# Kernel optimization log

Measured on AMD Instinct MI355X. Metric: run time of the kernel, lower is better.

## Reference

```python
import jax, jax.numpy as jnp
import numpy as np

EPS = 1e-7
LN_EPS = 1e-5

N_NODES = 50000
N_EDGES = 1600000
D = 128
L = 3


def layer_norm(h, scale, bias):
    mu = jnp.mean(h, axis=-1, keepdims=True)
    var = jnp.var(h, axis=-1, keepdims=True)
    return (h - mu) * jax.lax.rsqrt(var + LN_EPS) * scale + bias


def gen_conv(h, src, dst, edge_attr, W1, b1, W2, b2, beta, n_nodes):
    # message: ReLU(x_j + edge_attr) + eps   -> [E, D]
    msg = jax.nn.relu(h[src] + edge_attr) + EPS
    # softmax aggregation over incoming edges of each dst node, per feature
    s = beta * msg
    m = jax.ops.segment_max(s, dst, num_segments=n_nodes)  # [N, D]
    e = jnp.exp(s - m[dst])
    den = jax.ops.segment_sum(e, dst, num_segments=n_nodes)  # [N, D]
    alpha = e / den[dst]
    aggr = jax.ops.segment_sum(alpha * msg, dst, num_segments=n_nodes)  # [N, D]
    # MLP(x + aggr): D -> 2D -> D
    out = h + aggr
    out = jax.nn.relu(out @ W1 + b1)
    return out @ W2 + b2


def setup_inputs() -> dict:
    key = jax.random.key(0)
    ks = jax.random.split(key, 8)
    x = jax.random.normal(ks[0], (N_NODES, D), dtype=jnp.float32)
    edge_index = jax.random.randint(ks[1], (2, N_EDGES), 0, N_NODES, dtype=jnp.int64)
    edge_attr = jax.random.normal(ks[2], (N_EDGES, D), dtype=jnp.float32)
    return {
        "x": x,
        "edge_index": edge_index,
        "edge_attr": edge_attr,
        "ln_scale": jnp.ones((L, D), jnp.float32),
        "ln_bias": jnp.zeros((L, D), jnp.float32),
        "W1": jax.random.normal(ks[3], (L, D, 2 * D), jnp.float32) * 0.05,
        "b1": jnp.zeros((L, 2 * D), jnp.float32),
        "W2": jax.random.normal(ks[4], (L, 2 * D, D), jnp.float32) * 0.05,
        "b2": jnp.zeros((L, D), jnp.float32),
        "beta": jnp.ones((L,), jnp.float32),
        "lnf_scale": jnp.ones((D,), jnp.float32),
        "lnf_bias": jnp.zeros((D,), jnp.float32),
        "Wout": jax.random.normal(ks[5], (D, 1), jnp.float32) * 0.05,
        "bout": jnp.zeros((1,), jnp.float32),
    }


def reference(x, edge_index, edge_attr, ln_scale, ln_bias, W1, b1, W2, b2, beta,
              lnf_scale, lnf_bias, Wout, bout):
    src, dst = edge_index[0], edge_index[1]
    n = x.shape[0]
    # res+ DeeperGCN: first conv raw, then LN -> ReLU -> conv + residual
    h = gen_conv(x, src, dst, edge_attr, W1[0], b1[0], W2[0], b2[0], beta[0], n)
    for i in range(1, L):
        hn = jax.nn.relu(layer_norm(h, ln_scale[i], ln_bias[i]))
        h = gen_conv(hn, src, dst, edge_attr, W1[i], b1[i], W2[i], b2[i], beta[i], n) + h
    h = jax.nn.relu(layer_norm(h, lnf_scale, lnf_bias))
    return h @ Wout + bout
```

## Files before the change

kernel.cpp:

```cpp
#include <hip/hip_runtime.h>
#include <hip/hip_bf16.h>
#include <cstddef>

#define N_NODES 50000
#define N_EDGES 1600000
#define D 128
#define TWO_D 256
#define L 3
#define EPS 1e-7f
#define LN_EPS 1e-5f

typedef __attribute__((ext_vector_type(8))) short short8;
typedef __attribute__((ext_vector_type(4))) float f32x4;
typedef __attribute__((ext_vector_type(4))) unsigned u32x4;

__device__ __forceinline__ unsigned short f2bf(float f) {
    unsigned u = __float_as_uint(f);
    unsigned r = (u + 0x7fffu + ((u >> 16) & 1u)) >> 16;
    return (unsigned short)r;
}
__device__ __forceinline__ float bflo(unsigned u) { return __uint_as_float(u << 16); }
__device__ __forceinline__ float bfhi(unsigned u) { return __uint_as_float(u & 0xffff0000u); }
__device__ __forceinline__ unsigned bfpack(float lo, float hi) {
    return (unsigned)f2bf(lo) | ((unsigned)f2bf(hi) << 16);
}


__global__ __launch_bounds__(256) void hist_kernel(const int* __restrict__ ei, int* __restrict__ deg) {
    int idx = blockIdx.x * blockDim.x + threadIdx.x;
    int stride = gridDim.x * blockDim.x;
    for (int e = idx; e < N_EDGES; e += stride)
        atomicAdd(&deg[ei[N_EDGES + e]], 1);
}

__global__ __launch_bounds__(256) void scanA_kernel(const int* __restrict__ deg, int* __restrict__ part,
                                                    int* __restrict__ bsum) {
    __shared__ int wsum[4];
    int b = blockIdx.x, t = threadIdx.x;
    int lane = t & 63, wid = t >> 6;
    int base = b * 1024 + t * 4;
    int v0 = 0, v1 = 0, v2 = 0, v3 = 0;
    if (base + 0 < N_NODES) v0 = deg[base + 0];
    if (base + 1 < N_NODES) v1 = deg[base + 1];
    if (base + 2 < N_NODES) v2 = deg[base + 2];
    if (base + 3 < N_NODES) v3 = deg[base + 3];
    int s0 = v0, s1 = s0 + v1, s2 = s1 + v2, s3 = s2 + v3;
    int inc = s3;
    for (int off = 1; off < 64; off <<= 1) {
        int u = __shfl_up(inc, off);
        if (lane >= off) inc += u;
    }
    if (lane == 63) wsum[wid] = inc;
    __syncthreads();
    int woff = 0;
    for (int w = 0; w < wid; ++w) woff += wsum[w];
    int excl = woff + inc - s3;
    if (base + 0 < N_NODES) part[base + 0] = excl + s0;
    if (base + 1 < N_NODES) part[base + 1] = excl + s1;
    if (base + 2 < N_NODES) part[base + 2] = excl + s2;
    if (base + 3 < N_NODES) part[base + 3] = excl + s3;
    if (t == 255) bsum[b] = woff + inc;
}

__global__ __launch_bounds__(64) void scanB_kernel(int* __restrict__ bsum, int nb) {
    int lane = threadIdx.x;
    int v = (lane < nb) ? bsum[lane] : 0;
    int inc = v;
    for (int off = 1; off < 64; off <<= 1) {
        int u = __shfl_up(inc, off);
        if (lane >= off) inc += u;
    }
    if (lane < nb) bsum[lane] = inc - v;
}

__global__ __launch_bounds__(256) void scanC_kernel(const int* __restrict__ part, const int* __restrict__ bsum,
                                                    int* __restrict__ rowptr, int* __restrict__ cursor) {
    int i = blockIdx.x * blockDim.x + threadIdx.x;
    if (i >= N_NODES) return;
    rowptr[i + 1] = part[i] + bsum[i >> 10];
    cursor[i] = 0;
    if (i == 0) rowptr[0] = 0;
}

__global__ __launch_bounds__(256) void scatter_kernel(const int* __restrict__ ei, const int* __restrict__ rowptr,
                                                      int* __restrict__ cursor, int2* __restrict__ es2) {
    int idx = blockIdx.x * blockDim.x + threadIdx.x;
    int stride = gridDim.x * blockDim.x;
    for (int e = idx; e < N_EDGES; e += stride) {
        int dn = ei[N_EDGES + e];
        int pos = atomicAdd(&cursor[dn], 1);
        es2[rowptr[dn] + pos] = make_int2(ei[e], e);
    }
}

__global__ __launch_bounds__(256) void x2bf_kernel(const float* __restrict__ x, ushort2* __restrict__ xb) {
    int i = blockIdx.x * blockDim.x + threadIdx.x;
    if (i >= N_NODES * (D / 2)) return;
    float2 v = *(const float2*)(x + (size_t)i * 2);
    ushort2 o;
    o.x = f2bf(v.x);
    o.y = f2bf(v.y);
    xb[i] = o;
}

__global__ __launch_bounds__(256) void pack_w_kernel(const float* __restrict__ W1, const float* __restrict__ W2,
                                                     ushort* __restrict__ w1p, ushort* __restrict__ w2p) {
    int tid = blockIdx.x * 256 + threadIdx.x;
    if (tid >= 3 * 65536) return;
    int layer = tid >> 16, t2 = tid & 65535;
    if (t2 < 32768) {
        int j = t2 & 7, l = (t2 >> 3) & 63, kk = (t2 >> 9) & 3, ct = t2 >> 11;
        int k = kk * 32 + (l >> 4) * 8 + j, n = ct * 16 + (l & 15);
        w1p[(size_t)layer * 32768 + t2] = f2bf(W1[(size_t)layer * 32768 + k * 256 + n]);
    } else {
        int t3 = t2 - 32768;
        int j = t3 & 7, l = (t3 >> 3) & 63, kk = (t3 >> 9) & 7, ct = t3 >> 12;
        int k = kk * 32 + (l >> 4) * 8 + j, n = ct * 16 + (l & 15);
        w2p[(size_t)layer * 32768 + t3] = f2bf(W2[(size_t)layer * 32768 + k * 128 + n]);
    }
}


template <int PREP>
__global__ __launch_bounds__(256) void aggregate_kernel(const uint4* __restrict__ nodeb,
                                                        const float* __restrict__ ea,
                                                        ushort* __restrict__ eab,
                                                        const int* __restrict__ rowptr,
                                                        const int2* __restrict__ es2,
                                                        const float* __restrict__ beta, int layer,
                                                        ushort* __restrict__ preb) {
    int wid = threadIdx.x >> 6, lane = threadIdx.x & 63;
    int d = blockIdx.x * 4 + wid;
    if (d >= N_NODES) return;
    int e8 = lane >> 3;
    int f8 = lane & 7;
    float bet = beta[layer];
    int j0 = rowptr[d], j1 = rowptr[d + 1];
    int deg = j1 - j0;

    uint4 r0 = nodeb[(size_t)d * 16 + f8 * 2 + 0];
    uint4 r1 = nodeb[(size_t)d * 16 + f8 * 2 + 1];

    float se[16], sm[16];
#pragma unroll
    for (int i = 0; i < 16; ++i) { se[i] = 0.f; sm[i] = 0.f; }

    if (deg > 0) {
        int2 mp = (j0 + lane < j1) ? es2[j0 + lane] : make_int2(0, 0);
        bool small = (deg <= 64);
#pragma unroll 4
        for (int j = j0; j < j1; j += 8) {
            int e = j + e8;
            bool valid = e < j1;
            int ec = valid ? e : j1 - 1;
            int s, eid;
            if (small) {
                s   = __shfl(mp.x, ec - j0);
                eid = __shfl(mp.y, ec - j0);
            } else {
                int2 p = es2[ec];
                s = p.x; eid = p.y;
            }
            uint4 h0 = nodeb[(size_t)s * 16 + f8 * 2 + 0];
            uint4 h1 = nodeb[(size_t)s * 16 + f8 * 2 + 1];
            const unsigned* hu = (const unsigned*)&h0;
            const unsigned* hv = (const unsigned*)&h1;
            float vm = valid ? 1.f : 0.f;
            float af[16];
            if (PREP) {
                const float* ep = ea + (size_t)eid * D + f8 * 16;
                f32x4 fa0 = *(const f32x4*)(ep + 0);
                f32x4 fa1 = *(const f32x4*)(ep + 4);
                f32x4 fa2 = *(const f32x4*)(ep + 8);
                f32x4 fa3 = *(const f32x4*)(ep + 12);
#pragma unroll
                for (int q = 0; q < 4; ++q) {
                    af[q] = fa0[q];
                    af[4 + q] = fa1[q];
                    af[8 + q] = fa2[q];
                    af[12 + q] = fa3[q];
                }
                if (valid) {
                    u32x4 o0, o1;
                    o0[0] = bfpack(af[0], af[1]);  o0[1] = bfpack(af[2], af[3]);
                    o0[2] = bfpack(af[4], af[5]);  o0[3] = bfpack(af[6], af[7]);
                    o1[0] = bfpack(af[8], af[9]);  o1[1] = bfpack(af[10], af[11]);
                    o1[2] = bfpack(af[12], af[13]); o1[3] = bfpack(af[14], af[15]);
                    u32x4* dst = (u32x4*)(eab + (size_t)ec * D + f8 * 16);
                    dst[0] = o0;
                    dst[1] = o1;
                }
            } else {
                const u32x4* ap = (const u32x4*)(eab + (size_t)ec * D + f8 * 16);
                u32x4 a0 = ap[0];
                u32x4 a1 = ap[1];
#pragma unroll
                for (int q = 0; q < 4; ++q) {
                    af[q * 2 + 0] = bflo(a0[q]); af[q * 2 + 1] = bfhi(a0[q]);
                    af[8 + q * 2 + 0] = bflo(a1[q]); af[8 + q * 2 + 1] = bfhi(a1[q]);
                }
            }
#pragma unroll
            for (int q = 0; q < 4; ++q) {
                float m0 = fmaxf(bflo(hu[q]) + af[q * 2 + 0], 0.f) + EPS;
                float m1 = fmaxf(bfhi(hu[q]) + af[q * 2 + 1], 0.f) + EPS;
                float ee0 = __expf(bet * m0) * vm;
                float ee1 = __expf(bet * m1) * vm;
                se[q * 2 + 0] += ee0; sm[q * 2 + 0] = fmaf(ee0, m0, sm[q * 2 + 0]);
                se[q * 2 + 1] += ee1; sm[q * 2 + 1] = fmaf(ee1, m1, sm[q * 2 + 1]);
            }
#pragma unroll
            for (int q = 0; q < 4; ++q) {
                float m0 = fmaxf(bflo(hv[q]) + af[8 + q * 2 + 0], 0.f) + EPS;
                float m1 = fmaxf(bfhi(hv[q]) + af[8 + q * 2 + 1], 0.f) + EPS;
                float ee0 = __expf(bet * m0) * vm;
                float ee1 = __expf(bet * m1) * vm;
                se[8 + q * 2 + 0] += ee0; sm[8 + q * 2 + 0] = fmaf(ee0, m0, sm[8 + q * 2 + 0]);
                se[8 + q * 2 + 1] += ee1; sm[8 + q * 2 + 1] = fmaf(ee1, m1, sm[8 + q * 2 + 1]);
            }
        }
    }

#pragma unroll
    for (int off = 8; off < 64; off <<= 1) {
#pragma unroll
        for (int i = 0; i < 16; ++i) {
            se[i] += __shfl_xor(se[i], off);
            sm[i] += __shfl_xor(sm[i], off);
        }
    }

    if (e8 == 0) {
        const unsigned* ru = (const unsigned*)&r0;
        const unsigned* rv = (const unsigned*)&r1;
        float v[16];
#pragma unroll
        for (int q = 0; q < 4; ++q) {
            v[q * 2 + 0] = bflo(ru[q]) + (se[q * 2 + 0] > 0.f ? sm[q * 2 + 0] / se[q * 2 + 0] : 0.f);
            v[q * 2 + 1] = bfhi(ru[q]) + (se[q * 2 + 1] > 0.f ? sm[q * 2 + 1] / se[q * 2 + 1] : 0.f);
            v[8 + q * 2 + 0] = bflo(rv[q]) + (se[8 + q * 2 + 0] > 0.f ? sm[8 + q * 2 + 0] / se[8 + q * 2 + 0] : 0.f);
            v[8 + q * 2 + 1] = bfhi(rv[q]) + (se[8 + q * 2 + 1] > 0.f ? sm[8 + q * 2 + 1] / se[8 + q * 2 + 1] : 0.f);
        }
        uint4 o0, o1;
        o0.x = bfpack(v[0], v[1]);   o0.y = bfpack(v[2], v[3]);
        o0.z = bfpack(v[4], v[5]);   o0.w = bfpack(v[6], v[7]);
        o1.x = bfpack(v[8], v[9]);   o1.y = bfpack(v[10], v[11]);
        o1.z = bfpack(v[12], v[13]); o1.w = bfpack(v[14], v[15]);
        uint4* dst = (uint4*)(preb + (size_t)d * D + f8 * 16);
        dst[0] = o0;
        dst[1] = o1;
    }
}


__global__ __launch_bounds__(256) void mlp_kernel(const ushort* __restrict__ preb,
                                                  const ushort* __restrict__ w1p, const float* __restrict__ b1,
                                                  const ushort* __restrict__ w2p, const float* __restrict__ b2,
                                                  const float* __restrict__ res,
                                                  float* __restrict__ h_out,
                                                  const float* __restrict__ ln_s, const float* __restrict__ ln_b,
                                                  ushort* __restrict__ hnb_out,
                                                  const float* __restrict__ Wout, const float* __restrict__ bout,
                                                  float* __restrict__ out, int mode) {
    __shared__ ushort hid[32][264];
    __shared__ float hid2[32][132];
    int t = threadIdx.x;
    int lane = t & 63, w = t >> 6;
    int rt = w & 1, ch = w >> 1;
    int node0 = blockIdx.x * 32;
    int l15 = lane & 15, l4 = lane >> 4;

    f32x4 acc[8];
#pragma unroll
    for (int ct = 0; ct < 8; ++ct) {
        float bb = b1[ch * 128 + ct * 16 + l15];
        f32x4 v = {bb, bb, bb, bb};
        acc[ct] = v;
    }
    const ushort* aprow = preb + (size_t)(node0 + rt * 16 + l15) * D + l4 * 8;
    const short8* w1f = (const short8*)w1p;
#pragma unroll
    for (int kk = 0; kk < 4; ++kk) {
        short8 a = *(const short8*)(aprow + kk * 32);
#pragma unroll
        for (int ct = 0; ct < 8; ++ct) {
            int ctg = ch * 8 + ct;
            short8 b = w1f[(ctg * 4 + kk) * 64 + lane];
            acc[ct] = __builtin_amdgcn_mfma_f32_16x16x32_bf16(a, b, acc[ct], 0, 0, 0);
        }
    }
#pragma unroll
    for (int ct = 0; ct < 8; ++ct) {
        int feat = ch * 128 + ct * 16 + l15;
        int row = rt * 16 + l4 * 4;
#pragma unroll
        for (int r = 0; r < 4; ++r)
            hid[row + r][feat] = f2bf(fmaxf(acc[ct][r], 0.f));
    }
    __syncthreads();

    f32x4 acc2[4];
#pragma unroll
    for (int ct = 0; ct < 4; ++ct) {
        f32x4 z = {0.f, 0.f, 0.f, 0.f};
        acc2[ct] = z;
    }
    const ushort* ahrow = &hid[rt * 16 + l15][l4 * 8];
    const short8* w2f = (const short8*)w2p;
#pragma unroll
    for (int kk = 0; kk < 8; ++kk) {
        short8 a = *(const short8*)(ahrow + kk * 32);
#pragma unroll
        for (int ct = 0; ct < 4; ++ct) {
            int ctg = ch * 4 + ct;
            short8 b = w2f[(ctg * 8 + kk) * 64 + lane];
            acc2[ct] = __builtin_amdgcn_mfma_f32_16x16x32_bf16(a, b, acc2[ct], 0, 0, 0);
        }
    }
#pragma unroll
    for (int ct = 0; ct < 4; ++ct) {
        int feat = ch * 64 + ct * 16 + l15;
        int row = rt * 16 + l4 * 4;
#pragma unroll
        for (int r = 0; r < 4; ++r)
            hid2[row + r][feat] = acc2[ct][r];
    }
    __syncthreads();

    int f4 = (t & 31) * 4;
    int ng = t >> 5;
    float4 b2v = *(const float4*)(b2 + f4);
#pragma unroll 1
    for (int n = 0; n < 4; ++n) {
        int nl = ng * 4 + n;
        int node = node0 + nl;
        bool valid = node < N_NODES;
        float4 v = *(float4*)&hid2[nl][f4];
        v.x += b2v.x; v.y += b2v.y; v.z += b2v.z; v.w += b2v.w;
        if (res != nullptr && valid) {
            float4 rv = *(const float4*)(res + (size_t)node * D + f4);
            v.x += rv.x; v.y += rv.y; v.z += rv.z; v.w += rv.w;
        }
        if (mode < 2 && valid) *(float4*)(h_out + (size_t)node * D + f4) = v;

        float s = v.x + v.y + v.z + v.w;
        for (int off = 16; off; off >>= 1) s += __shfl_xor(s, off);
        float mu = s * (1.0f / D);
        float dx = v.x - mu, dy = v.y - mu, dz = v.z - mu, dw = v.w - mu;
        float vs = dx * dx + dy * dy + dz * dz + dw * dw;
        for (int off = 16; off; off >>= 1) vs += __shfl_xor(vs, off);
        float r = rsqrtf(vs * (1.0f / D) + LN_EPS);
        float4 sc = *(const float4*)(ln_s + f4);
        float4 bi = *(const float4*)(ln_b + f4);
        float y0 = fmaxf(dx * r * sc.x + bi.x, 0.f);
        float y1 = fmaxf(dy * r * sc.y + bi.y, 0.f);
        float y2 = fmaxf(dz * r * sc.z + bi.z, 0.f);
        float y3 = fmaxf(dw * r * sc.w + bi.w, 0.f);
        if (mode < 2) {
            if (valid) {
                ushort4 hb;
                hb.x = f2bf(y0); hb.y = f2bf(y1); hb.z = f2bf(y2); hb.w = f2bf(y3);
                *(ushort4*)(hnb_out + (size_t)node * D + f4) = hb;
            }
        } else {
            float4 wv = *(const float4*)(Wout + f4);
            float dot = y0 * wv.x + y1 * wv.y + y2 * wv.z + y3 * wv.w;
            for (int off = 16; off; off >>= 1) dot += __shfl_xor(dot, off);
            if ((t & 31) == 0 && valid) out[node] = dot + bout[0];
        }
    }
}


extern "C" void kernel_launch(void* const* d_in, const int* in_sizes, int n_in,
                              void* d_out, int out_size, void* d_ws, size_t ws_size,
                              hipStream_t stream) {
    const float* x        = (const float*)d_in[0];
    const int*   ei       = (const int*)d_in[1];
    const float* ea       = (const float*)d_in[2];
    const float* ln_scale = (const float*)d_in[3];
    const float* ln_bias  = (const float*)d_in[4];
    const float* W1       = (const float*)d_in[5];
    const float* b1       = (const float*)d_in[6];
    const float* W2       = (const float*)d_in[7];
    const float* b2       = (const float*)d_in[8];
    const float* beta     = (const float*)d_in[9];
    const float* lnf_s    = (const float*)d_in[10];
    const float* lnf_b    = (const float*)d_in[11];
    const float* Wout     = (const float*)d_in[12];
    const float* bout     = (const float*)d_in[13];
    float* out = (float*)d_out;

    char* w = (char*)d_ws;
    float*  h    = (float*)w;  w += (size_t)N_NODES * D * 4;
    ushort* preb = (ushort*)w; w += (size_t)N_NODES * D * 2;
    ushort* hnb  = (ushort*)w; w += (size_t)N_NODES * D * 2;
    ushort* xb   = (ushort*)w; w += (size_t)N_NODES * D * 2;
    ushort* eab  = (ushort*)w; w += (size_t)N_EDGES * D * 2;
    int2* es2   = (int2*)w;  w += (size_t)N_EDGES * 8;
    ushort* w1p = (ushort*)w; w += (size_t)3 * 32768 * 2;
    ushort* w2p = (ushort*)w; w += (size_t)3 * 32768 * 2;
    int* deg    = (int*)w;   w += (size_t)N_NODES * 4;
    int* part   = (int*)w;   w += (size_t)50176 * 4;
    int* rowptr = (int*)w;   w += (size_t)(N_NODES + 1) * 4;
    int* cursor = (int*)w;   w += (size_t)N_NODES * 4;
    int* bsum   = (int*)w;   w += (size_t)64 * 4;

    const int NB = (N_NODES + 1023) / 1024;

    hipMemsetAsync(deg, 0, (size_t)N_NODES * 4, stream);
    hist_kernel<<<2048, 256, 0, stream>>>(ei, deg);
    scanA_kernel<<<NB, 256, 0, stream>>>(deg, part, bsum);
    scanB_kernel<<<1, 64, 0, stream>>>(bsum, NB);
    scanC_kernel<<<(N_NODES + 255) / 256, 256, 0, stream>>>(part, bsum, rowptr, cursor);
    scatter_kernel<<<2048, 256, 0, stream>>>(ei, rowptr, cursor, es2);
    x2bf_kernel<<<(N_NODES * (D / 2) + 255) / 256, 256, 0, stream>>>(x, (ushort2*)xb);
    pack_w_kernel<<<768, 256, 0, stream>>>(W1, W2, w1p, w2p);

    const int grid_rows = (N_NODES + 3) / 4;
    const int grid_gemm = (N_NODES + 31) / 32;

    for (int layer = 0; layer < L; ++layer) {
        const uint4* nodeb = (const uint4*)((layer == 0) ? xb : hnb);
        if (layer == 0)
            aggregate_kernel<1><<<grid_rows, 256, 0, stream>>>(nodeb, ea, eab, rowptr, es2, beta, layer, preb);
        else
            aggregate_kernel<0><<<grid_rows, 256, 0, stream>>>(nodeb, ea, eab, rowptr, es2, beta, layer, preb);

        if (layer < L - 1) {
            mlp_kernel<<<grid_gemm, 256, 0, stream>>>(preb,
                                                      w1p + (size_t)layer * 32768, b1 + (size_t)layer * TWO_D,
                                                      w2p + (size_t)layer * 32768, b2 + (size_t)layer * D,
                                                      layer == 0 ? nullptr : h, h,
                                                      ln_scale + (size_t)(layer + 1) * D,
                                                      ln_bias + (size_t)(layer + 1) * D,
                                                      hnb, nullptr, nullptr, nullptr, layer == 0 ? 0 : 1);
        } else {
            mlp_kernel<<<grid_gemm, 256, 0, stream>>>(preb,
                                                      w1p + (size_t)layer * 32768, b1 + (size_t)layer * TWO_D,
                                                      w2p + (size_t)layer * 32768, b2 + (size_t)layer * D,
                                                      h, nullptr,
                                                      lnf_s, lnf_b, nullptr,
                                                      Wout, bout, out, 2);
        }
    }
}
```

Baseline: 776.6 us.

## Merge setup kernels, read fp32 x directly in layer 0, use nontemporal edge loads

Folds the weight packing into the degree-histogram kernel and the block-sum scan into the final scan kernel, and drops the x-to-bf16 conversion kernel, which cuts several launches. The first aggregation now gathers fp32 x directly, doubling its gather bytes in exchange for skipping the conversion pass. Edge-attribute reads and the bf16 edge-attribute writes use nontemporal hints to limit cache pollution. The layer-0 path also now works on full-precision x rather than a bf16 copy.

Result: slower. 896.7 us (+15.5%).

```diff
diff --git a/kernel.cpp b/kernel.cpp
--- a/kernel.cpp
+++ b/kernel.cpp
@@ -26,11 +26,29 @@
 }
 
 
-__global__ __launch_bounds__(256) void hist_kernel(const int* __restrict__ ei, int* __restrict__ deg) {
-    int idx = blockIdx.x * blockDim.x + threadIdx.x;
-    int stride = gridDim.x * blockDim.x;
-    for (int e = idx; e < N_EDGES; e += stride)
-        atomicAdd(&deg[ei[N_EDGES + e]], 1);
+__global__ __launch_bounds__(256) void build_kernel(const int* __restrict__ ei, int* __restrict__ deg,
+                                                    const float* __restrict__ W1, const float* __restrict__ W2,
+                                                    ushort* __restrict__ w1p, ushort* __restrict__ w2p) {
+    int b = blockIdx.x;
+    if (b < 768) {
+        int tid = b * 256 + threadIdx.x;
+        int layer = tid >> 16, t2 = tid & 65535;
+        if (t2 < 32768) {
+            int j = t2 & 7, l = (t2 >> 3) & 63, kk = (t2 >> 9) & 3, ct = t2 >> 11;
+            int k = kk * 32 + (l >> 4) * 8 + j, n = ct * 16 + (l & 15);
+            w1p[(size_t)layer * 32768 + t2] = f2bf(W1[(size_t)layer * 32768 + k * 256 + n]);
+        } else {
+            int t3 = t2 - 32768;
+            int j = t3 & 7, l = (t3 >> 3) & 63, kk = (t3 >> 9) & 7, ct = t3 >> 12;
+            int k = kk * 32 + (l >> 4) * 8 + j, n = ct * 16 + (l & 15);
+            w2p[(size_t)layer * 32768 + t3] = f2bf(W2[(size_t)layer * 32768 + k * 128 + n]);
+        }
+    } else {
+        int idx = (b - 768) * 256 + threadIdx.x;
+        int stride = 2048 * 256;
+        for (int e = idx; e < N_EDGES; e += stride)
+            atomicAdd(&deg[ei[N_EDGES + e]], 1);
+    }
 }
 
 __global__ __launch_bounds__(256) void scanA_kernel(const int* __restrict__ deg, int* __restrict__ part,
@@ -62,22 +80,23 @@
     if (t == 255) bsum[b] = woff + inc;
 }
 
-__global__ __launch_bounds__(64) void scanB_kernel(int* __restrict__ bsum, int nb) {
-    int lane = threadIdx.x;
-    int v = (lane < nb) ? bsum[lane] : 0;
-    int inc = v;
-    for (int off = 1; off < 64; off <<= 1) {
-        int u = __shfl_up(inc, off);
-        if (lane >= off) inc += u;
-    }
-    if (lane < nb) bsum[lane] = inc - v;
-}
-
-__global__ __launch_bounds__(256) void scanC_kernel(const int* __restrict__ part, const int* __restrict__ bsum,
-                                                    int* __restrict__ rowptr, int* __restrict__ cursor) {
-    int i = blockIdx.x * blockDim.x + threadIdx.x;
+__global__ __launch_bounds__(256) void scan2_kernel(const int* __restrict__ part, const int* __restrict__ bsum,
+                                                    int nb, int* __restrict__ rowptr, int* __restrict__ cursor) {
+    __shared__ int excl[64];
+    int t = threadIdx.x;
+    if (t < 64) {
+        int v = (t < nb) ? bsum[t] : 0;
+        int inc = v;
+        for (int off = 1; off < 64; off <<= 1) {
+            int u = __shfl_up(inc, off);
+            if (t >= off) inc += u;
+        }
+        excl[t] = inc - v;
+    }
+    __syncthreads();
+    int i = blockIdx.x * blockDim.x + t;
     if (i >= N_NODES) return;
-    rowptr[i + 1] = part[i] + bsum[i >> 10];
+    rowptr[i + 1] = part[i] + excl[i >> 10];
     cursor[i] = 0;
     if (i == 0) rowptr[0] = 0;
 }
@@ -93,36 +112,10 @@
     }
 }
 
-__global__ __launch_bounds__(256) void x2bf_kernel(const float* __restrict__ x, ushort2* __restrict__ xb) {
-    int i = blockIdx.x * blockDim.x + threadIdx.x;
-    if (i >= N_NODES * (D / 2)) return;
-    float2 v = *(const float2*)(x + (size_t)i * 2);
-    ushort2 o;
-    o.x = f2bf(v.x);
-    o.y = f2bf(v.y);
-    xb[i] = o;
-}
-
-__global__ __launch_bounds__(256) void pack_w_kernel(const float* __restrict__ W1, const float* __restrict__ W2,
-                                                     ushort* __restrict__ w1p, ushort* __restrict__ w2p) {
-    int tid = blockIdx.x * 256 + threadIdx.x;
-    if (tid >= 3 * 65536) return;
-    int layer = tid >> 16, t2 = tid & 65535;
-    if (t2 < 32768) {
-        int j = t2 & 7, l = (t2 >> 3) & 63, kk = (t2 >> 9) & 3, ct = t2 >> 11;
-        int k = kk * 32 + (l >> 4) * 8 + j, n = ct * 16 + (l & 15);
-        w1p[(size_t)layer * 32768 + t2] = f2bf(W1[(size_t)layer * 32768 + k * 256 + n]);
-    } else {
-        int t3 = t2 - 32768;
-        int j = t3 & 7, l = (t3 >> 3) & 63, kk = (t3 >> 9) & 7, ct = t3 >> 12;
-        int k = kk * 32 + (l >> 4) * 8 + j, n = ct * 16 + (l & 15);
-        w2p[(size_t)layer * 32768 + t3] = f2bf(W2[(size_t)layer * 32768 + k * 128 + n]);
-    }
-}
-
 
 template <int PREP>
 __global__ __launch_bounds__(256) void aggregate_kernel(const uint4* __restrict__ nodeb,
+                                                        const float* __restrict__ xf,
                                                         const float* __restrict__ ea,
                                                         ushort* __restrict__ eab,
                                                         const int* __restrict__ rowptr,
@@ -137,9 +130,6 @@
     float bet = beta[layer];
     int j0 = rowptr[d], j1 = rowptr[d + 1];
     int deg = j1 - j0;
-
-    uint4 r0 = nodeb[(size_t)d * 16 + f8 * 2 + 0];
-    uint4 r1 = nodeb[(size_t)d * 16 + f8 * 2 + 1];
 
     float se[16], sm[16];
 #pragma unroll
@@ -161,24 +151,23 @@
                 int2 p = es2[ec];
                 s = p.x; eid = p.y;
             }
-            uint4 h0 = nodeb[(size_t)s * 16 + f8 * 2 + 0];
-            uint4 h1 = nodeb[(size_t)s * 16 + f8 * 2 + 1];
-            const unsigned* hu = (const unsigned*)&h0;
-            const unsigned* hv = (const unsigned*)&h1;
             float vm = valid ? 1.f : 0.f;
-            float af[16];
+            float hf[16], af[16];
             if (PREP) {
+                const float* hp = xf + (size_t)s * D + f8 * 16;
+                f32x4 hh0 = *(const f32x4*)(hp + 0);
+                f32x4 hh1 = *(const f32x4*)(hp + 4);
+                f32x4 hh2 = *(const f32x4*)(hp + 8);
+                f32x4 hh3 = *(const f32x4*)(hp + 12);
                 const float* ep = ea + (size_t)eid * D + f8 * 16;
-                f32x4 fa0 = *(const f32x4*)(ep + 0);
-                f32x4 fa1 = *(const f32x4*)(ep + 4);
-                f32x4 fa2 = *(const f32x4*)(ep + 8);
-                f32x4 fa3 = *(const f32x4*)(ep + 12);
+                f32x4 fa0 = __builtin_nontemporal_load((const f32x4*)(ep + 0));
+                f32x4 fa1 = __builtin_nontemporal_load((const f32x4*)(ep + 4));
+                f32x4 fa2 = __builtin_nontemporal_load((const f32x4*)(ep + 8));
+                f32x4 fa3 = __builtin_nontemporal_load((const f32x4*)(ep + 12));
 #pragma unroll
                 for (int q = 0; q < 4; ++q) {
-                    af[q] = fa0[q];
-                    af[4 + q] = fa1[q];
-                    af[8 + q] = fa2[q];
-                    af[12 + q] = fa3[q];
+                    hf[q] = hh0[q]; hf[4 + q] = hh1[q]; hf[8 + q] = hh2[q]; hf[12 + q] = hh3[q];
+                    af[q] = fa0[q]; af[4 + q] = fa1[q]; af[8 + q] = fa2[q]; af[12 + q] = fa3[q];
                 }
                 if (valid) {
                     u32x4 o0, o1;
@@ -187,36 +176,39 @@
                     o1[0] = bfpack(af[8], af[9]);  o1[1] = bfpack(af[10], af[11]);
                     o1[2] = bfpack(af[12], af[13]); o1[3] = bfpack(af[14], af[15]);
                     u32x4* dst = (u32x4*)(eab + (size_t)ec * D + f8 * 16);
-                    dst[0] = o0;
-                    dst[1] = o1;
+                    __builtin_nontemporal_store(o0, dst + 0);
+                    __builtin_nontemporal_store(o1, dst + 1);
                 }
             } else {
+                uint4 h0 = nodeb[(size_t)s * 16 + f8 * 2 + 0];
+                uint4 h1 = nodeb[(size_t)s * 16 + f8 * 2 + 1];
+                const unsigned* hu = (const unsigned*)&h0;
+                const unsigned* hv = (const unsigned*)&h1;
                 const u32x4* ap = (const u32x4*)(eab + (size_t)ec * D + f8 * 16);
-                u32x4 a0 = ap[0];
-                u32x4 a1 = ap[1];
+                u32x4 a0 = __builtin_nontemporal_load(ap + 0);
+                u32x4 a1 = __builtin_nontemporal_load(ap + 1);
 #pragma unroll
                 for (int q = 0; q < 4; ++q) {
+                    hf[q * 2 + 0] = bflo(hu[q]); hf[q * 2 + 1] = bfhi(hu[q]);
+                    hf[8 + q * 2 + 0] = bflo(hv[q]); hf[8 + q * 2 + 1] = bfhi(hv[q]);
                     af[q * 2 + 0] = bflo(a0[q]); af[q * 2 + 1] = bfhi(a0[q]);
                     af[8 + q * 2 + 0] = bflo(a1[q]); af[8 + q * 2 + 1] = bfhi(a1[q]);
                 }
             }
-#pragma unroll
-            for (int q = 0; q < 4; ++q) {
-                float m0 = fmaxf(bflo(hu[q]) + af[q * 2 + 0], 0.f) + EPS;
-                float m1 = fmaxf(bfhi(hu[q]) + af[q * 2 + 1], 0.f) + EPS;
-                float ee0 = __expf(bet * m0) * vm;
-                float ee1 = __expf(bet * m1) * vm;
-                se[q * 2 + 0] += ee0; sm[q * 2 + 0] = fmaf(ee0, m0, sm[q * 2 + 0]);
-                se[q * 2 + 1] += ee1; sm[q * 2 + 1] = fmaf(ee1, m1, sm[q * 2 + 1]);
-            }
-#pragma unroll
-            for (int q = 0; q < 4; ++q) {
-                float m0 = fmaxf(bflo(hv[q]) + af[8 + q * 2 + 0], 0.f) + EPS;
-                float m1 = fmaxf(bfhi(hv[q]) + af[8 + q * 2 + 1], 0.f) + EPS;
-                float ee0 = __expf(bet * m0) * vm;
-                float ee1 = __expf(bet * m1) * vm;
-                se[8 + q * 2 + 0] += ee0; sm[8 + q * 2 + 0] = fmaf(ee0, m0, sm[8 + q * 2 + 0]);
-                se[8 + q * 2 + 1] += ee1; sm[8 + q * 2 + 1] = fmaf(ee1, m1, sm[8 + q * 2 + 1]);
+            if (PREP) {
+#pragma unroll
+                for (int q = 0; q < 16; ++q) {
+                    float m = fmaxf(hf[q] + af[q], 0.f) + EPS;
+                    float ee = __expf(bet * m) * vm;
+                    se[q] += ee; sm[q] = fmaf(ee, m, sm[q]);
+                }
+            } else {
+#pragma unroll
+                for (int q = 0; q < 16; ++q) {
+                    float m = fmaxf(hf[q] + af[q], 0.f) + EPS;
+                    float ee = __expf(bet * m) * vm;
+                    se[q] += ee; sm[q] = fmaf(ee, m, sm[q]);
+                }
             }
         }
     }
@@ -231,24 +223,43 @@
     }
 
     if (e8 == 0) {
-        const unsigned* ru = (const unsigned*)&r0;
-        const unsigned* rv = (const unsigned*)&r1;
         float v[16];
-#pragma unroll
-        for (int q = 0; q < 4; ++q) {
-            v[q * 2 + 0] = bflo(ru[q]) + (se[q * 2 + 0] > 0.f ? sm[q * 2 + 0] / se[q * 2 + 0] : 0.f);
-            v[q * 2 + 1] = bfhi(ru[q]) + (se[q * 2 + 1] > 0.f ? sm[q * 2 + 1] / se[q * 2 + 1] : 0.f);
-            v[8 + q * 2 + 0] = bflo(rv[q]) + (se[8 + q * 2 + 0] > 0.f ? sm[8 + q * 2 + 0] / se[8 + q * 2 + 0] : 0.f);
-            v[8 + q * 2 + 1] = bfhi(rv[q]) + (se[8 + q * 2 + 1] > 0.f ? sm[8 + q * 2 + 1] / se[8 + q * 2 + 1] : 0.f);
-        }
-        uint4 o0, o1;
-        o0.x = bfpack(v[0], v[1]);   o0.y = bfpack(v[2], v[3]);
-        o0.z = bfpack(v[4], v[5]);   o0.w = bfpack(v[6], v[7]);
-        o1.x = bfpack(v[8], v[9]);   o1.y = bfpack(v[10], v[11]);
-        o1.z = bfpack(v[12], v[13]); o1.w = bfpack(v[14], v[15]);
-        uint4* dst = (uint4*)(preb + (size_t)d * D + f8 * 16);
-        dst[0] = o0;
-        dst[1] = o1;
+        if (PREP) {
+            const float* rp = xf + (size_t)d * D + f8 * 16;
+#pragma unroll
+            for (int q = 0; q < 16; ++q) {
+                float rv = rp[q];
+                v[q] = rv + (se[q] > 0.f ? sm[q] / se[q] : 0.f);
+            }
+            uint4 o0, o1;
+            o0.x = bfpack(v[0], v[1]);   o0.y = bfpack(v[2], v[3]);
+            o0.z = bfpack(v[4], v[5]);   o0.w = bfpack(v[6], v[7]);
+            o1.x = bfpack(v[8], v[9]);   o1.y = bfpack(v[10], v[11]);
+            o1.z = bfpack(v[12], v[13]); o1.w = bfpack(v[14], v[15]);
+            uint4* dst = (uint4*)(preb + (size_t)d * D + f8 * 16);
+            dst[0] = o0;
+            dst[1] = o1;
+        } else {
+            uint4 r0 = nodeb[(size_t)d * 16 + f8 * 2 + 0];
+            uint4 r1 = nodeb[(size_t)d * 16 + f8 * 2 + 1];
+            const unsigned* ru = (const unsigned*)&r0;
+            const unsigned* rv = (const unsigned*)&r1;
+#pragma unroll
+            for (int q = 0; q < 4; ++q) {
+                v[q * 2 + 0] = bflo(ru[q]) + (se[q * 2 + 0] > 0.f ? sm[q * 2 + 0] / se[q * 2 + 0] : 0.f);
+                v[q * 2 + 1] = bfhi(ru[q]) + (se[q * 2 + 1] > 0.f ? sm[q * 2 + 1] / se[q * 2 + 1] : 0.f);
+                v[8 + q * 2 + 0] = bflo(rv[q]) + (se[8 + q * 2 + 0] > 0.f ? sm[8 + q * 2 + 0] / se[8 + q * 2 + 0] : 0.f);
+                v[8 + q * 2 + 1] = bfhi(rv[q]) + (se[8 + q * 2 + 1] > 0.f ? sm[8 + q * 2 + 1] / se[8 + q * 2 + 1] : 0.f);
+            }
+            uint4 o0, o1;
+            o0.x = bfpack(v[0], v[1]);   o0.y = bfpack(v[2], v[3]);
+            o0.z = bfpack(v[4], v[5]);   o0.w = bfpack(v[6], v[7]);
+            o1.x = bfpack(v[8], v[9]);   o1.y = bfpack(v[10], v[11]);
+            o1.z = bfpack(v[12], v[13]); o1.w = bfpack(v[14], v[15]);
+            uint4* dst = (uint4*)(preb + (size_t)d * D + f8 * 16);
+            dst[0] = o0;
+            dst[1] = o1;
+        }
     }
 }
 
@@ -395,7 +406,6 @@
     float*  h    = (float*)w;  w += (size_t)N_NODES * D * 4;
     ushort* preb = (ushort*)w; w += (size_t)N_NODES * D * 2;
     ushort* hnb  = (ushort*)w; w += (size_t)N_NODES * D * 2;
-    ushort* xb   = (ushort*)w; w += (size_t)N_NODES * D * 2;
     ushort* eab  = (ushort*)w; w += (size_t)N_EDGES * D * 2;
     int2* es2   = (int2*)w;  w += (size_t)N_EDGES * 8;
     ushort* w1p = (ushort*)w; w += (size_t)3 * 32768 * 2;
@@ -409,23 +419,20 @@
     const int NB = (N_NODES + 1023) / 1024;
 
     hipMemsetAsync(deg, 0, (size_t)N_NODES * 4, stream);
-    hist_kernel<<<2048, 256, 0, stream>>>(ei, deg);
+    build_kernel<<<2816, 256, 0, stream>>>(ei, deg, W1, W2, w1p, w2p);
     scanA_kernel<<<NB, 256, 0, stream>>>(deg, part, bsum);
-    scanB_kernel<<<1, 64, 0, stream>>>(bsum, NB);
-    scanC_kernel<<<(N_NODES + 255) / 256, 256, 0, stream>>>(part, bsum, rowptr, cursor);
+    scan2_kernel<<<(N_NODES + 255) / 256, 256, 0, stream>>>(part, bsum, NB, rowptr, cursor);
     scatter_kernel<<<2048, 256, 0, stream>>>(ei, rowptr, cursor, es2);
-    x2bf_kernel<<<(N_NODES * (D / 2) + 255) / 256, 256, 0, stream>>>(x, (ushort2*)xb);
-    pack_w_kernel<<<768, 256, 0, stream>>>(W1, W2, w1p, w2p);
 
     const int grid_rows = (N_NODES + 3) / 4;
     const int grid_gemm = (N_NODES + 31) / 32;
 
     for (int layer = 0; layer < L; ++layer) {
-        const uint4* nodeb = (const uint4*)((layer == 0) ? xb : hnb);
         if (layer == 0)
-            aggregate_kernel<1><<<grid_rows, 256, 0, stream>>>(nodeb, ea, eab, rowptr, es2, beta, layer, preb);
+            aggregate_kernel<1><<<grid_rows, 256, 0, stream>>>(nullptr, x, ea, eab, rowptr, es2, beta, layer, preb);
         else
-            aggregate_kernel<0><<<grid_rows, 256, 0, stream>>>(nodeb, ea, eab, rowptr, es2, beta, layer, preb);
+            aggregate_kernel<0><<<grid_rows, 256, 0, stream>>>((const uint4*)hnb, nullptr, ea, eab,
+                                                               rowptr, es2, beta, layer, preb);
 
         if (layer < L - 1) {
             mlp_kernel<<<grid_gemm, 256, 0, stream>>>(preb,
```
